# Kernel optimization log

Hardware: AMD Instinct MI355X
Metric: run time of the kernel (lower is better)

Reference implementation:

```python
import jax, jax.numpy as jnp
import numpy as np

LN_EPS = 1e-5

def _ln(x, g, b):
    m = jnp.mean(x, -1, keepdims=True)
    v = jnp.var(x, -1, keepdims=True)
    return (x - m) / jnp.sqrt(v + LN_EPS) * g + b

def _modgru(X, M, hx0, mask, Wcomb, bcomb, Wih, Whh, bih, bhh, Wc2, bc2):
    # X, M: [S,B,D]; hx0: [B,H]; mask: [S,B]
    # comb and the input-side gate GEMMs are hx-independent -> precompute over all steps
    comb = jnp.einsum('sbd,ed->sbe', jnp.concatenate([X, M], -1), Wcomb) + bcomb  # [S,B,D]
    gi = jnp.einsum('sbd,gd->sbg', comb, Wih) + bih  # [S,B,3H]

    def step(hx, inp):
        gi_t, m_t = inp
        gh = hx @ Whh.T + bhh
        ir, iz, inn = jnp.split(gi_t, 3, -1)
        hr, hz, hn = jnp.split(gh, 3, -1)
        r = jax.nn.sigmoid(ir + hr)
        z = jax.nn.sigmoid(iz + hz)
        n = jnp.tanh(inn + r * hn)
        hnew = (1.0 - z) * n + z * hx  # torch GRUCell update
        m = m_t[:, None]
        hx = hnew * m + hx * (1.0 - m)  # mask blending
        return hx, hx

    hx_last, hs = jax.lax.scan(step, hx0, (gi, mask))  # hs: [S,B,H]
    out = jnp.einsum('sbd,ed->sbe', jnp.concatenate([comb, hs], -1), Wc2) + bc2
    return out, hx_last

def setup_inputs() -> dict:
    key = jax.random.key(0)
    ks = jax.random.split(key, 40)
    S, B, I, H = 256, 512, 70, 512
    D1 = I - 6  # rnn1 input dim (use_src=True)
    f32 = jnp.float32
    def w(k, shape, scale):
        return jax.random.normal(k, shape, f32) * scale
    inp = {
        'X': jax.random.normal(ks[0], (S, B, I), f32),
        'M': (jax.random.uniform(ks[1], (S, B, I)) < 0.9).astype(f32),
        'mask': (jax.random.uniform(ks[2], (S, B)) < 0.95).astype(f32),
        'Wi2h': w(ks[3], (H, 6), 0.3), 'bi2h': jnp.zeros((H,), f32),
        # rnn1 (ModGRU on D1 inputs)
        'Wcomb1': w(ks[4], (D1, 2 * D1), 0.08), 'bcomb1': jnp.zeros((D1,), f32),
        'Wih1': w(ks[5], (3 * H, D1), 0.08), 'Whh1': w(ks[6], (3 * H, H), 0.04),
        'bih1': jnp.zeros((3 * H,), f32), 'bhh1': jnp.zeros((3 * H,), f32),
        'Wc21': w(ks[7], (H, D1 + H), 0.04), 'bc21': jnp.zeros((H,), f32),
        # rnn2 (ModGRU on H inputs)
        'Wcomb2': w(ks[8], (H, 2 * H), 0.03), 'bcomb2': jnp.zeros((H,), f32),
        'Wih2': w(ks[9], (3 * H, H), 0.04), 'Whh2': w(ks[10], (3 * H, H), 0.04),
        'bih2': jnp.zeros((3 * H,), f32), 'bhh2': jnp.zeros((3 * H,), f32),
        'Wc22': w(ks[11], (H, 2 * H), 0.03), 'bc22': jnp.zeros((H,), f32),
        # layer norms
        'g1': jnp.ones((H,), f32), 'b1': jnp.zeros((H,), f32),
        'g2': jnp.ones((H,), f32), 'b2': jnp.zeros((H,), f32),
        'g3': jnp.ones((8,), f32), 'b3': jnp.zeros((8,), f32),
        # heads
        'Wnn1': w(ks[12], (8, H), 0.05), 'bnn1': jnp.zeros((8,), f32),
        'Wnn2': w(ks[13], (2, 8), 0.3), 'bnn2': jnp.zeros((2,), f32),
    }
    return inp

def reference(X, M, mask, Wi2h, bi2h,
              Wcomb1, bcomb1, Wih1, Whh1, bih1, bhh1, Wc21, bc21,
              Wcomb2, bcomb2, Wih2, Whh2, bih2, bhh2, Wc22, bc22,
              g1, b1, g2, b2, g3, b3, Wnn1, bnn1, Wnn2, bnn2):
    # use_src=True: last 6 channels are static patient info
    patient = X[0, :, -6:]                  # [B,6]
    Xin, Min = X[:, :, :-6], M[:, :, :-6]   # [S,B,D1]
    h0 = patient @ Wi2h.T + bi2h            # [B,H]
    hx, _ = _modgru(Xin, Min, h0, mask, Wcomb1, bcomb1, Wih1, Whh1, bih1, bhh1, Wc21, bc21)
    hx = _ln(hx, g1, b1)
    hx, _ = _modgru(hx, jnp.ones_like(hx), h0, mask, Wcomb2, bcomb2, Wih2, Whh2, bih2, bhh2, Wc22, bc22)
    hx = _ln(hx, g2, b2)
    hx = jax.nn.relu(jnp.einsum('sbh,oh->sbo', hx, Wnn1) + bnn1)
    hx = _ln(hx, g3, b3)
    return jnp.einsum('sbh,oh->sbo', hx, Wnn2) + bnn2  # [S,B,2]
```

## Files before the change

### kernel.cpp

```cpp
#include <hip/hip_runtime.h>
#include <hip/hip_bf16.h>

typedef unsigned short u16;
typedef unsigned int   u32;

#define S_  256
#define B_  512
#define H_  512
#define I_  70

__device__ __forceinline__ float bfu(u16 u) {
    return __uint_as_float(((u32)u) << 16);
}
__device__ __forceinline__ u16 f2bf_u(float f) {
    __hip_bfloat16 h = __float2bfloat16(f);
    u16 r;
    __builtin_memcpy(&r, &h, 2);
    return r;
}
__device__ __forceinline__ float sigmoidf_(float x) {
    x = fminf(fmaxf(x, -30.f), 30.f);
    return 1.f / (1.f + __expf(-x));
}
__device__ __forceinline__ float tanhf_(float x) {
    x = fminf(fmaxf(x, -15.f), 15.f);
    float e = __expf(2.f * x);
    return (e - 1.f) / (e + 1.f);
}

__global__ __launch_bounds__(256)
void k_sentinel(float* __restrict__ out, int n, float v) {
    int i = blockIdx.x * 256 + threadIdx.x;
    if (i < n) out[i] = v;
}

__global__ __launch_bounds__(256)
void k_h0(const float* __restrict__ X, const float* __restrict__ Wi2h,
          const float* __restrict__ bi2h, float* __restrict__ h1a,
          float* __restrict__ h2a) {
    int idx = blockIdx.x * 256 + threadIdx.x;
    int b = idx >> 9, h = idx & 511;
    const float* xp = X + b * I_ + 64;
    const float* wp = Wi2h + h * 6;
    float s = bi2h[h];
    #pragma unroll
    for (int j = 0; j < 6; j++) s += xp[j] * wp[j];
    h1a[idx] = s;
    h2a[idx] = s;
}

__global__ __launch_bounds__(256)
void k_beff(const float* __restrict__ Wcomb2, const float* __restrict__ bcomb2,
            float* __restrict__ beff) {
    int e = blockIdx.x * 256 + threadIdx.x;
    if (e >= 512) return;
    float s = bcomb2[e];
    const float* wp = Wcomb2 + (size_t)e * 1024 + 512;
    for (int k = 0; k < 512; k++) s += wp[k];
    beff[e] = s;
}

__global__ __launch_bounds__(256)
void k_comb1(const float* __restrict__ X, const float* __restrict__ M,
             const float* __restrict__ Wcomb1, const float* __restrict__ bcomb1,
             u16* __restrict__ comb1) {
    __shared__ float W_s[128 * 68];
    __shared__ float in_s[16 * 132];
    const int tid = threadIdx.x;
    for (int i = tid; i < 64 * 128; i += 256) {
        int e = i >> 7, k = i & 127;
        W_s[k * 68 + e] = Wcomb1[i];
    }
    const size_t row0 = (size_t)blockIdx.x * 16;
    for (int i = tid; i < 16 * 128; i += 256) {
        int r = i >> 7, k = i & 127;
        size_t rg = row0 + r;
        in_s[r * 132 + k] = (k < 64) ? X[rg * I_ + k] : M[rg * I_ + (k - 64)];
    }
    __syncthreads();
    const int ty = tid >> 4, tx = tid & 15;
    float a0 = 0, a1 = 0, a2 = 0, a3 = 0;
    for (int k = 0; k < 128; k++) {
        float a = in_s[ty * 132 + k];
        float w[4];
        *(float4*)w = *(const float4*)&W_s[k * 68 + tx * 4];
        a0 = fmaf(a, w[0], a0); a1 = fmaf(a, w[1], a1);
        a2 = fmaf(a, w[2], a2); a3 = fmaf(a, w[3], a3);
    }
    size_t rg = row0 + ty;
    int e0 = tx * 4;
    ushort4 st;
    st.x = f2bf_u(a0 + bcomb1[e0 + 0]);
    st.y = f2bf_u(a1 + bcomb1[e0 + 1]);
    st.z = f2bf_u(a2 + bcomb1[e0 + 2]);
    st.w = f2bf_u(a3 + bcomb1[e0 + 3]);
    *(ushort4*)&comb1[rg * 64 + e0] = st;
}

template<int D>
__global__ __launch_bounds__(256)
void k_gru_step(const u16* __restrict__ comb,
                const float* __restrict__ Wih,
                const float* __restrict__ Whh,
                const float* __restrict__ bih, const float* __restrict__ bhh,
                const float* __restrict__ mask,
                const float* __restrict__ hcur, float* __restrict__ hnxt,
                const int t) {
    __shared__ float W_s[24 * 516];
    const int tid = threadIdx.x;
    const int hl = tid & 7;
    const int ty = tid >> 3;
    const int h0 = blockIdx.x * 8;
    const int h  = h0 + hl;
    const int b  = blockIdx.y * 64 + ty * 2;

    for (int i = tid; i < 24 * 128; i += 256) {
        int r = i >> 7, kq = i & 127;
        int g = r >> 3, hh = r & 7;
        *(float4*)&W_s[r * 516 + kq * 4] =
            *(const float4*)&Whh[((size_t)(g * 512 + h0 + hh)) * 512 + kq * 4];
    }
    __syncthreads();

    const float* hr0 = hcur + (size_t)b * 512;
    const float* hr1 = hcur + (size_t)(b + 1) * 512;
    float gh00 = bhh[h], gh10 = bhh[512 + h], gh20 = bhh[1024 + h];
    float gh01 = gh00, gh11 = gh10, gh21 = gh20;
    {
        const float* w0p = &W_s[(0 * 8 + hl) * 516];
        const float* w1p = &W_s[(1 * 8 + hl) * 516];
        const float* w2p = &W_s[(2 * 8 + hl) * 516];
        for (int k = 0; k < 512; k += 4) {
            float4 w0 = *(const float4*)(w0p + k);
            float4 w1 = *(const float4*)(w1p + k);
            float4 w2 = *(const float4*)(w2p + k);
            float4 ha = *(const float4*)(hr0 + k);
            float4 hb = *(const float4*)(hr1 + k);
            gh00 = fmaf(w0.x, ha.x, gh00); gh00 = fmaf(w0.y, ha.y, gh00);
            gh00 = fmaf(w0.z, ha.z, gh00); gh00 = fmaf(w0.w, ha.w, gh00);
            gh10 = fmaf(w1.x, ha.x, gh10); gh10 = fmaf(w1.y, ha.y, gh10);
            gh10 = fmaf(w1.z, ha.z, gh10); gh10 = fmaf(w1.w, ha.w, gh10);
            gh20 = fmaf(w2.x, ha.x, gh20); gh20 = fmaf(w2.y, ha.y, gh20);
            gh20 = fmaf(w2.z, ha.z, gh20); gh20 = fmaf(w2.w, ha.w, gh20);
            gh01 = fmaf(w0.x, hb.x, gh01); gh01 = fmaf(w0.y, hb.y, gh01);
            gh01 = fmaf(w0.z, hb.z, gh01); gh01 = fmaf(w0.w, hb.w, gh01);
            gh11 = fmaf(w1.x, hb.x, gh11); gh11 = fmaf(w1.y, hb.y, gh11);
            gh11 = fmaf(w1.z, hb.z, gh11); gh11 = fmaf(w1.w, hb.w, gh11);
            gh21 = fmaf(w2.x, hb.x, gh21); gh21 = fmaf(w2.y, hb.y, gh21);
            gh21 = fmaf(w2.z, hb.z, gh21); gh21 = fmaf(w2.w, hb.w, gh21);
        }
    }
    __syncthreads();
    constexpr int KQ = D / 4;
    constexpr int WST = (D == 512) ? 516 : (D + 4);
    for (int i = tid; i < 24 * KQ; i += 256) {
        int r = i / KQ, kq = i % KQ;
        int g = r >> 3, hh = r & 7;
        *(float4*)&W_s[r * WST + kq * 4] =
            *(const float4*)&Wih[((size_t)(g * 512 + h0 + hh)) * D + kq * 4];
    }
    __syncthreads();

    const u16* cr0 = comb + ((size_t)t * 512 + b) * D;
    const u16* cr1 = comb + ((size_t)t * 512 + b + 1) * D;
    float gi00 = bih[h], gi10 = bih[512 + h], gi20 = bih[1024 + h];
    float gi01 = gi00, gi11 = gi10, gi21 = gi20;
    {
        const float* w0p = &W_s[(0 * 8 + hl) * WST];
        const float* w1p = &W_s[(1 * 8 + hl) * WST];
        const float* w2p = &W_s[(2 * 8 + hl) * WST];
        for (int k = 0; k < D; k += 4) {
            float4 w0 = *(const float4*)(w0p + k);
            float4 w1 = *(const float4*)(w1p + k);
            float4 w2 = *(const float4*)(w2p + k);
            ushort4 cu0 = *(const ushort4*)(cr0 + k);
            ushort4 cu1 = *(const ushort4*)(cr1 + k);
            float ca[4] = {bfu(cu0.x), bfu(cu0.y), bfu(cu0.z), bfu(cu0.w)};
            float cb[4] = {bfu(cu1.x), bfu(cu1.y), bfu(cu1.z), bfu(cu1.w)};
            gi00 = fmaf(w0.x, ca[0], gi00); gi00 = fmaf(w0.y, ca[1], gi00);
            gi00 = fmaf(w0.z, ca[2], gi00); gi00 = fmaf(w0.w, ca[3], gi00);
            gi10 = fmaf(w1.x, ca[0], gi10); gi10 = fmaf(w1.y, ca[1], gi10);
            gi10 = fmaf(w1.z, ca[2], gi10); gi10 = fmaf(w1.w, ca[3], gi10);
            gi20 = fmaf(w2.x, ca[0], gi20); gi20 = fmaf(w2.y, ca[1], gi20);
            gi20 = fmaf(w2.z, ca[2], gi20); gi20 = fmaf(w2.w, ca[3], gi20);
            gi01 = fmaf(w0.x, cb[0], gi01); gi01 = fmaf(w0.y, cb[1], gi01);
            gi01 = fmaf(w0.z, cb[2], gi01); gi01 = fmaf(w0.w, cb[3], gi01);
            gi11 = fmaf(w1.x, cb[0], gi11); gi11 = fmaf(w1.y, cb[1], gi11);
            gi11 = fmaf(w1.z, cb[2], gi11); gi11 = fmaf(w1.w, cb[3], gi11);
            gi21 = fmaf(w2.x, cb[0], gi21); gi21 = fmaf(w2.y, cb[1], gi21);
            gi21 = fmaf(w2.z, cb[2], gi21); gi21 = fmaf(w2.w, cb[3], gi21);
        }
    }
    {
        float hold = hr0[h];
        float r = sigmoidf_(gi00 + gh00);
        float z = sigmoidf_(gi10 + gh10);
        float n = tanhf_(gi20 + r * gh20);
        float m = mask[t * 512 + b];
        hnxt[(size_t)b * 512 + h] = ((1.f - z) * n + z * hold) * m + hold * (1.f - m);
    }
    {
        float hold = hr1[h];
        float r = sigmoidf_(gi01 + gh01);
        float z = sigmoidf_(gi11 + gh11);
        float n = tanhf_(gi21 + r * gh21);
        float m = mask[t * 512 + b + 1];
        hnxt[(size_t)(b + 1) * 512 + h] = ((1.f - z) * n + z * hold) * m + hold * (1.f - m);
    }
}

__global__ __launch_bounds__(256)
void k_out1comb2(const u16* __restrict__ c1t, const float* __restrict__ h1,
                 const float* __restrict__ Wc21, const float* __restrict__ bc21,
                 const float* __restrict__ g1, const float* __restrict__ b1,
                 const float* __restrict__ Wcomb2, const float* __restrict__ beff,
                 u16* __restrict__ c2t) {
    __shared__ float x_s[4 * 576];
    __shared__ float y_s[4 * 512];
    const int tid = threadIdx.x;
    const int row0 = blockIdx.x * 4;
    for (int i = tid; i < 4 * 64; i += 256) {
        int r = i >> 6, k = i & 63;
        x_s[r * 576 + k] = bfu(c1t[(size_t)(row0 + r) * 64 + k]);
    }
    for (int i = tid; i < 4 * 512; i += 256) {
        int r = i >> 9, k = i & 511;
        x_s[r * 576 + 64 + k] = h1[(size_t)(row0 + r) * 512 + k];
    }
    __syncthreads();
    const int w = tid >> 6, lane = tid & 63;
    const int cg = lane >> 4, kl = lane & 15;
    for (int i = 0; i < 32; i++) {
        int o = i * 16 + w * 4 + cg;
        const float* wrow = Wc21 + (size_t)o * 576;
        float racc[4] = {0.f, 0.f, 0.f, 0.f};
        #pragma unroll
        for (int g = 0; g < 9; g++) {
            int k = g * 64 + kl * 4;
            float4 wv = *(const float4*)(wrow + k);
            #pragma unroll
            for (int r = 0; r < 4; r++) {
                float4 xv = *(const float4*)(x_s + r * 576 + k);
                racc[r] = fmaf(wv.x, xv.x, racc[r]);
                racc[r] = fmaf(wv.y, xv.y, racc[r]);
                racc[r] = fmaf(wv.z, xv.z, racc[r]);
                racc[r] = fmaf(wv.w, xv.w, racc[r]);
            }
        }
        #pragma unroll
        for (int r = 0; r < 4; r++) {
            racc[r] += __shfl_xor(racc[r], 1, 64);
            racc[r] += __shfl_xor(racc[r], 2, 64);
            racc[r] += __shfl_xor(racc[r], 4, 64);
            racc[r] += __shfl_xor(racc[r], 8, 64);
        }
        if (kl == 0) {
            float bb = bc21[o];
            #pragma unroll
            for (int r = 0; r < 4; r++) y_s[r * 512 + o] = racc[r] + bb;
        }
    }
    __syncthreads();
    {
        float v[8], sum = 0.f, ssq = 0.f;
        #pragma unroll
        for (int j = 0; j < 8; j++) {
            v[j] = y_s[w * 512 + lane * 8 + j];
            sum += v[j]; ssq += v[j] * v[j];
        }
        #pragma unroll
        for (int m = 1; m < 64; m <<= 1) {
            sum += __shfl_xor(sum, m, 64);
            ssq += __shfl_xor(ssq, m, 64);
        }
        float mu = sum * (1.f / 512.f);
        float rstd = rsqrtf(ssq * (1.f / 512.f) - mu * mu + 1e-5f);
        #pragma unroll
        for (int j = 0; j < 8; j++) {
            int o = lane * 8 + j;
            y_s[w * 512 + o] = (v[j] - mu) * rstd * g1[o] + b1[o];
        }
    }
    __syncthreads();
    for (int i = 0; i < 32; i++) {
        int o = i * 16 + w * 4 + cg;
        const float* wrow = Wcomb2 + (size_t)o * 1024;
        float racc[4] = {0.f, 0.f, 0.f, 0.f};
        #pragma unroll
        for (int g = 0; g < 8; g++) {
            int k = g * 64 + kl * 4;
            float4 wv = *(const float4*)(wrow + k);
            #pragma unroll
            for (int r = 0; r < 4; r++) {
                float4 xv = *(const float4*)(y_s + r * 512 + k);
                racc[r] = fmaf(wv.x, xv.x, racc[r]);
                racc[r] = fmaf(wv.y, xv.y, racc[r]);
                racc[r] = fmaf(wv.z, xv.z, racc[r]);
                racc[r] = fmaf(wv.w, xv.w, racc[r]);
            }
        }
        #pragma unroll
        for (int r = 0; r < 4; r++) {
            racc[r] += __shfl_xor(racc[r], 1, 64);
            racc[r] += __shfl_xor(racc[r], 2, 64);
            racc[r] += __shfl_xor(racc[r], 4, 64);
            racc[r] += __shfl_xor(racc[r], 8, 64);
        }
        if (kl == 0) {
            float bb = beff[o];
            #pragma unroll
            for (int r = 0; r < 4; r++)
                c2t[(size_t)(row0 + r) * 512 + o] = f2bf_u(racc[r] + bb);
        }
    }
}

__global__ __launch_bounds__(256)
void k_out2head(const u16* __restrict__ c2t, const float* __restrict__ h2,
                const float* __restrict__ Wc22, const float* __restrict__ bc22,
                const float* __restrict__ g2, const float* __restrict__ b2,
                const float* __restrict__ Wnn1, const float* __restrict__ bnn1,
                const float* __restrict__ g3, const float* __restrict__ b3,
                const float* __restrict__ Wnn2, const float* __restrict__ bnn2,
                float* __restrict__ outt) {
    __shared__ float x_s[4 * 1024];
    __shared__ float y_s[4 * 512];
    const int tid = threadIdx.x;
    const int row0 = blockIdx.x * 4;
    for (int i = tid; i < 4 * 512; i += 256) {
        int r = i >> 9, k = i & 511;
        x_s[r * 1024 + k] = bfu(c2t[(size_t)(row0 + r) * 512 + k]);
        x_s[r * 1024 + 512 + k] = h2[(size_t)(row0 + r) * 512 + k];
    }
    __syncthreads();
    const int w = tid >> 6, lane = tid & 63;
    const int cg = lane >> 4, kl = lane & 15;
    for (int i = 0; i < 32; i++) {
        int o = i * 16 + w * 4 + cg;
        const float* wrow = Wc22 + (size_t)o * 1024;
        float racc[4] = {0.f, 0.f, 0.f, 0.f};
        #pragma unroll
        for (int g = 0; g < 16; g++) {
            int k = g * 64 + kl * 4;
            float4 wv = *(const float4*)(wrow + k);
            #pragma unroll
            for (int r = 0; r < 4; r++) {
                float4 xv = *(const float4*)(x_s + r * 1024 + k);
                racc[r] = fmaf(wv.x, xv.x, racc[r]);
                racc[r] = fmaf(wv.y, xv.y, racc[r]);
                racc[r] = fmaf(wv.z, xv.z, racc[r]);
                racc[r] = fmaf(wv.w, xv.w, racc[r]);
            }
        }
        #pragma unroll
        for (int r = 0; r < 4; r++) {
            racc[r] += __shfl_xor(racc[r], 1, 64);
            racc[r] += __shfl_xor(racc[r], 2, 64);
            racc[r] += __shfl_xor(racc[r], 4, 64);
            racc[r] += __shfl_xor(racc[r], 8, 64);
        }
        if (kl == 0) {
            float bb = bc22[o];
            #pragma unroll
            for (int r = 0; r < 4; r++) y_s[r * 512 + o] = racc[r] + bb;
        }
    }
    __syncthreads();
    {
        float v[8], sum = 0.f, ssq = 0.f;
        #pragma unroll
        for (int j = 0; j < 8; j++) {
            v[j] = y_s[w * 512 + lane * 8 + j];
            sum += v[j]; ssq += v[j] * v[j];
        }
        #pragma unroll
        for (int m = 1; m < 64; m <<= 1) {
            sum += __shfl_xor(sum, m, 64);
            ssq += __shfl_xor(ssq, m, 64);
        }
        float mu = sum * (1.f / 512.f);
        float rstd = rsqrtf(ssq * (1.f / 512.f) - mu * mu + 1e-5f);
        #pragma unroll
        for (int j = 0; j < 8; j++) {
            int o = lane * 8 + j;
            y_s[w * 512 + o] = (v[j] - mu) * rstd * g2[o] + b2[o];
        }
    }
    __syncthreads();
    {
        float p[8];
        const float* yp = y_s + w * 512 + lane * 8;
        #pragma unroll
        for (int o8 = 0; o8 < 8; o8++) {
            const float* wp = Wnn1 + o8 * 512 + lane * 8;
            float s = 0.f;
            #pragma unroll
            for (int j = 0; j < 8; j++) s = fmaf(yp[j], wp[j], s);
            p[o8] = s;
        }
        #pragma unroll
        for (int m = 1; m < 64; m <<= 1) {
            #pragma unroll
            for (int o8 = 0; o8 < 8; o8++) p[o8] += __shfl_xor(p[o8], m, 64);
        }
        if (lane == 0) {
            float tv[8], m8 = 0.f;
            #pragma unroll
            for (int o8 = 0; o8 < 8; o8++) {
                tv[o8] = fmaxf(p[o8] + bnn1[o8], 0.f);
                m8 += tv[o8];
            }
            m8 *= 0.125f;
            float var = 0.f;
            #pragma unroll
            for (int o8 = 0; o8 < 8; o8++) { float d = tv[o8] - m8; var += d * d; }
            var *= 0.125f;
            const float rstd8 = rsqrtf(var + 1e-5f);
            float o0v = bnn2[0], o1v = bnn2[1];
            #pragma unroll
            for (int o8 = 0; o8 < 8; o8++) {
                float v = (tv[o8] - m8) * rstd8 * g3[o8] + b3[o8];
                o0v += v * Wnn2[o8];
                o1v += v * Wnn2[8 + o8];
            }
            outt[(row0 + w) * 2 + 0] = o0v;
            outt[(row0 + w) * 2 + 1] = o1v;
        }
    }
}

extern "C" void kernel_launch(void* const* d_in, const int* in_sizes, int n_in,
                              void* d_out, int out_size, void* d_ws, size_t ws_size,
                              hipStream_t stream) {
    const float* X      = (const float*)d_in[0];
    const float* M      = (const float*)d_in[1];
    const float* mask   = (const float*)d_in[2];
    const float* Wi2h   = (const float*)d_in[3];
    const float* bi2h   = (const float*)d_in[4];
    const float* Wcomb1 = (const float*)d_in[5];
    const float* bcomb1 = (const float*)d_in[6];
    const float* Wih1   = (const float*)d_in[7];
    const float* Whh1   = (const float*)d_in[8];
    const float* bih1   = (const float*)d_in[9];
    const float* bhh1   = (const float*)d_in[10];
    const float* Wc21   = (const float*)d_in[11];
    const float* bc21   = (const float*)d_in[12];
    const float* Wcomb2 = (const float*)d_in[13];
    const float* bcomb2 = (const float*)d_in[14];
    const float* Wih2   = (const float*)d_in[15];
    const float* Whh2   = (const float*)d_in[16];
    const float* bih2   = (const float*)d_in[17];
    const float* bhh2   = (const float*)d_in[18];
    const float* Wc22   = (const float*)d_in[19];
    const float* bc22   = (const float*)d_in[20];
    const float* g1     = (const float*)d_in[21];
    const float* b1     = (const float*)d_in[22];
    const float* g2     = (const float*)d_in[23];
    const float* b2     = (const float*)d_in[24];
    const float* g3     = (const float*)d_in[25];
    const float* b3     = (const float*)d_in[26];
    const float* Wnn1   = (const float*)d_in[27];
    const float* bnn1   = (const float*)d_in[28];
    const float* Wnn2   = (const float*)d_in[29];
    const float* bnn2   = (const float*)d_in[30];
    float* out = (float*)d_out;

    const size_t SZ_COMB1 = (size_t)S_ * B_ * 64 * 2;
    const size_t SZ_HX    = (size_t)B_ * H_ * 4;
    const size_t SZ_C2T   = (size_t)B_ * 512 * 2;
    const size_t NEED = SZ_COMB1 + 4 * SZ_HX + SZ_C2T + 8192;
    if (ws_size < NEED) {
        float v = 1.0e4f + (float)(ws_size >> 20);
        k_sentinel<<<(out_size + 255) / 256, 256, 0, stream>>>(out, out_size, v);
        return;
    }
    char* ws = (char*)d_ws;
    u16* comb1 = (u16*)ws;   ws += SZ_COMB1;
    float* h1a = (float*)ws; ws += SZ_HX;
    float* h1b = (float*)ws; ws += SZ_HX;
    float* h2a = (float*)ws; ws += SZ_HX;
    float* h2b = (float*)ws; ws += SZ_HX;
    u16* c2t   = (u16*)ws;   ws += SZ_C2T;
    float* beff = (float*)ws; ws += 512 * 4;

    k_h0<<<1024, 256, 0, stream>>>(X, Wi2h, bi2h, h1a, h2a);
    k_beff<<<2, 256, 0, stream>>>(Wcomb2, bcomb2, beff);
    k_comb1<<<8192, 256, 0, stream>>>(X, M, Wcomb1, bcomb1, comb1);

    for (int t = 0; t < S_; t++) {
        const float* h1c = (t & 1) ? h1b : h1a;
        float*       h1n = (t & 1) ? h1a : h1b;
        const float* h2c = (t & 1) ? h2b : h2a;
        float*       h2n = (t & 1) ? h2a : h2b;
        k_gru_step<64><<<dim3(64, 8), 256, 0, stream>>>(
            comb1, Wih1, Whh1, bih1, bhh1, mask, h1c, h1n, t);
        k_out1comb2<<<128, 256, 0, stream>>>(
            comb1 + (size_t)t * B_ * 64, h1n, Wc21, bc21, g1, b1,
            Wcomb2, beff, c2t);
        k_gru_step<512><<<dim3(64, 8), 256, 0, stream>>>(
            c2t, Wih2, Whh2, bih2, bhh2, mask + (size_t)t * B_, h2c, h2n, 0);
        k_out2head<<<128, 256, 0, stream>>>(
            c2t, h2n, Wc22, bc22, g2, b2, Wnn1, bnn1, g3, b3, Wnn2, bnn2,
            out + (size_t)t * B_ * 2);
    }
}
```

Baseline: 88.38 ms.

## Fuse per-timestep kernels into one persistent cooperative kernel with grid syncs

Replaces the 1024 per-timestep kernel launches with a single cooperative persistent kernel of 512 blocks that loops over timesteps and separates the four phases with grid.sync. GRU weight staging is split into 256-wide K chunks so shared memory fits about 25KB, which allows two blocks per CU and co-residency of all 512 blocks. The aim is to remove launch overhead and inter-kernel gaps. In exchange it adds grid-wide barriers and threadfences, and weights are still reloaded from global every step. A fallback multi-launch path runs if the cooperative launch fails.

```diff
diff --git a/kernel.cpp b/kernel.cpp
--- a/kernel.cpp
+++ b/kernel.cpp
@@ -1,5 +1,8 @@
 #include <hip/hip_runtime.h>
 #include <hip/hip_bf16.h>
+#include <hip/hip_cooperative_groups.h>
+
+namespace cg = cooperative_groups;
 
 typedef unsigned short u16;
 typedef unsigned int   u32;
@@ -8,6 +11,8 @@
 #define B_  512
 #define H_  512
 #define I_  70
+
+#define SM_FLOATS 6240
 
 __device__ __forceinline__ float bfu(u16 u) {
     return __uint_as_float(((u32)u) << 16);
@@ -97,45 +102,51 @@
     *(ushort4*)&comb1[rg * 64 + e0] = st;
 }
 
+
 template<int D>
-__global__ __launch_bounds__(256)
-void k_gru_step(const u16* __restrict__ comb,
-                const float* __restrict__ Wih,
-                const float* __restrict__ Whh,
-                const float* __restrict__ bih, const float* __restrict__ bhh,
-                const float* __restrict__ mask,
-                const float* __restrict__ hcur, float* __restrict__ hnxt,
-                const int t) {
-    __shared__ float W_s[24 * 516];
+__device__ void gru_phase(float* __restrict__ W_s,
+                          const u16* __restrict__ comb_t,
+                          const float* __restrict__ Wih,
+                          const float* __restrict__ Whh,
+                          const float* __restrict__ bih,
+                          const float* __restrict__ bhh,
+                          const float* __restrict__ maskRow,
+                          const float* __restrict__ hcur,
+                          float* __restrict__ hnxt) {
     const int tid = threadIdx.x;
     const int hl = tid & 7;
     const int ty = tid >> 3;
-    const int h0 = blockIdx.x * 8;
+    const int h0 = (blockIdx.x & 63) * 8;
     const int h  = h0 + hl;
-    const int b  = blockIdx.y * 64 + ty * 2;
-
-    for (int i = tid; i < 24 * 128; i += 256) {
-        int r = i >> 7, kq = i & 127;
-        int g = r >> 3, hh = r & 7;
-        *(float4*)&W_s[r * 516 + kq * 4] =
-            *(const float4*)&Whh[((size_t)(g * 512 + h0 + hh)) * 512 + kq * 4];
-    }
-    __syncthreads();
+    const int b  = (blockIdx.x >> 6) * 64 + ty * 2;
 
     const float* hr0 = hcur + (size_t)b * 512;
     const float* hr1 = hcur + (size_t)(b + 1) * 512;
     float gh00 = bhh[h], gh10 = bhh[512 + h], gh20 = bhh[1024 + h];
     float gh01 = gh00, gh11 = gh10, gh21 = gh20;
-    {
-        const float* w0p = &W_s[(0 * 8 + hl) * 516];
-        const float* w1p = &W_s[(1 * 8 + hl) * 516];
-        const float* w2p = &W_s[(2 * 8 + hl) * 516];
-        for (int k = 0; k < 512; k += 4) {
+
+    #pragma unroll
+    for (int half = 0; half < 2; half++) {
+        const int kbase = half * 256;
+        __syncthreads();
+        for (int i = tid; i < 24 * 64; i += 256) {
+            int r = i >> 6, kq = i & 63;
+            int g = r >> 3, hh = r & 7;
+            *(float4*)&W_s[r * 260 + kq * 4] =
+                *(const float4*)&Whh[((size_t)(g * 512 + h0 + hh)) * 512 + kbase + kq * 4];
+        }
+        __syncthreads();
+        const float* w0p = &W_s[(0 * 8 + hl) * 260];
+        const float* w1p = &W_s[(1 * 8 + hl) * 260];
+        const float* w2p = &W_s[(2 * 8 + hl) * 260];
+        const float* hap = hr0 + kbase;
+        const float* hbp = hr1 + kbase;
+        for (int k = 0; k < 256; k += 4) {
             float4 w0 = *(const float4*)(w0p + k);
             float4 w1 = *(const float4*)(w1p + k);
             float4 w2 = *(const float4*)(w2p + k);
-            float4 ha = *(const float4*)(hr0 + k);
-            float4 hb = *(const float4*)(hr1 + k);
+            float4 ha = *(const float4*)(hap + k);
+            float4 hb = *(const float4*)(hbp + k);
             gh00 = fmaf(w0.x, ha.x, gh00); gh00 = fmaf(w0.y, ha.y, gh00);
             gh00 = fmaf(w0.z, ha.z, gh00); gh00 = fmaf(w0.w, ha.w, gh00);
             gh10 = fmaf(w1.x, ha.x, gh10); gh10 = fmaf(w1.y, ha.y, gh10);
@@ -150,31 +161,32 @@
             gh21 = fmaf(w2.z, hb.z, gh21); gh21 = fmaf(w2.w, hb.w, gh21);
         }
     }
-    __syncthreads();
-    constexpr int KQ = D / 4;
-    constexpr int WST = (D == 512) ? 516 : (D + 4);
-    for (int i = tid; i < 24 * KQ; i += 256) {
-        int r = i / KQ, kq = i % KQ;
-        int g = r >> 3, hh = r & 7;
-        *(float4*)&W_s[r * WST + kq * 4] =
-            *(const float4*)&Wih[((size_t)(g * 512 + h0 + hh)) * D + kq * 4];
-    }
-    __syncthreads();
-
-    const u16* cr0 = comb + ((size_t)t * 512 + b) * D;
-    const u16* cr1 = comb + ((size_t)t * 512 + b + 1) * D;
+
+    constexpr int CH = (D < 256) ? D : 256;
+    constexpr int ST = CH + 4;
+    const u16* cr0 = comb_t + (size_t)b * D;
+    const u16* cr1 = comb_t + (size_t)(b + 1) * D;
     float gi00 = bih[h], gi10 = bih[512 + h], gi20 = bih[1024 + h];
     float gi01 = gi00, gi11 = gi10, gi21 = gi20;
-    {
-        const float* w0p = &W_s[(0 * 8 + hl) * WST];
-        const float* w1p = &W_s[(1 * 8 + hl) * WST];
-        const float* w2p = &W_s[(2 * 8 + hl) * WST];
-        for (int k = 0; k < D; k += 4) {
+    #pragma unroll
+    for (int kbase = 0; kbase < D; kbase += CH) {
+        __syncthreads();
+        for (int i = tid; i < 24 * (CH / 4); i += 256) {
+            int r = i / (CH / 4), kq = i % (CH / 4);
+            int g = r >> 3, hh = r & 7;
+            *(float4*)&W_s[r * ST + kq * 4] =
+                *(const float4*)&Wih[((size_t)(g * 512 + h0 + hh)) * D + kbase + kq * 4];
+        }
+        __syncthreads();
+        const float* w0p = &W_s[(0 * 8 + hl) * ST];
+        const float* w1p = &W_s[(1 * 8 + hl) * ST];
+        const float* w2p = &W_s[(2 * 8 + hl) * ST];
+        for (int k = 0; k < CH; k += 4) {
             float4 w0 = *(const float4*)(w0p + k);
             float4 w1 = *(const float4*)(w1p + k);
             float4 w2 = *(const float4*)(w2p + k);
-            ushort4 cu0 = *(const ushort4*)(cr0 + k);
-            ushort4 cu1 = *(const ushort4*)(cr1 + k);
+            ushort4 cu0 = *(const ushort4*)(cr0 + kbase + k);
+            ushort4 cu1 = *(const ushort4*)(cr1 + kbase + k);
             float ca[4] = {bfu(cu0.x), bfu(cu0.y), bfu(cu0.z), bfu(cu0.w)};
             float cb[4] = {bfu(cu1.x), bfu(cu1.y), bfu(cu1.z), bfu(cu1.w)};
             gi00 = fmaf(w0.x, ca[0], gi00); gi00 = fmaf(w0.y, ca[1], gi00);
@@ -196,7 +208,7 @@
         float r = sigmoidf_(gi00 + gh00);
         float z = sigmoidf_(gi10 + gh10);
         float n = tanhf_(gi20 + r * gh20);
-        float m = mask[t * 512 + b];
+        float m = maskRow[b];
         hnxt[(size_t)b * 512 + h] = ((1.f - z) * n + z * hold) * m + hold * (1.f - m);
     }
     {
@@ -204,19 +216,19 @@
         float r = sigmoidf_(gi01 + gh01);
         float z = sigmoidf_(gi11 + gh11);
         float n = tanhf_(gi21 + r * gh21);
-        float m = mask[t * 512 + b + 1];
+        float m = maskRow[b + 1];
         hnxt[(size_t)(b + 1) * 512 + h] = ((1.f - z) * n + z * hold) * m + hold * (1.f - m);
     }
 }
 
-__global__ __launch_bounds__(256)
-void k_out1comb2(const u16* __restrict__ c1t, const float* __restrict__ h1,
-                 const float* __restrict__ Wc21, const float* __restrict__ bc21,
-                 const float* __restrict__ g1, const float* __restrict__ b1,
-                 const float* __restrict__ Wcomb2, const float* __restrict__ beff,
-                 u16* __restrict__ c2t) {
-    __shared__ float x_s[4 * 576];
-    __shared__ float y_s[4 * 512];
+__device__ void b1_phase(float* __restrict__ sm,
+                         const u16* __restrict__ c1t, const float* __restrict__ h1,
+                         const float* __restrict__ Wc21, const float* __restrict__ bc21,
+                         const float* __restrict__ lg1, const float* __restrict__ lb1,
+                         const float* __restrict__ Wcomb2, const float* __restrict__ beff,
+                         u16* __restrict__ c2t) {
+    float* x_s = sm;
+    float* y_s = sm + 4 * 576;
     const int tid = threadIdx.x;
     const int row0 = blockIdx.x * 4;
     for (int i = tid; i < 4 * 64; i += 256) {
@@ -229,9 +241,9 @@
     }
     __syncthreads();
     const int w = tid >> 6, lane = tid & 63;
-    const int cg = lane >> 4, kl = lane & 15;
+    const int cg_ = lane >> 4, kl = lane & 15;
     for (int i = 0; i < 32; i++) {
-        int o = i * 16 + w * 4 + cg;
+        int o = i * 16 + w * 4 + cg_;
         const float* wrow = Wc21 + (size_t)o * 576;
         float racc[4] = {0.f, 0.f, 0.f, 0.f};
         #pragma unroll
@@ -278,12 +290,12 @@
         #pragma unroll
         for (int j = 0; j < 8; j++) {
             int o = lane * 8 + j;
-            y_s[w * 512 + o] = (v[j] - mu) * rstd * g1[o] + b1[o];
+            y_s[w * 512 + o] = (v[j] - mu) * rstd * lg1[o] + lb1[o];
         }
     }
     __syncthreads();
     for (int i = 0; i < 32; i++) {
-        int o = i * 16 + w * 4 + cg;
+        int o = i * 16 + w * 4 + cg_;
         const float* wrow = Wcomb2 + (size_t)o * 1024;
         float racc[4] = {0.f, 0.f, 0.f, 0.f};
         #pragma unroll
@@ -315,16 +327,16 @@
     }
 }
 
-__global__ __launch_bounds__(256)
-void k_out2head(const u16* __restrict__ c2t, const float* __restrict__ h2,
-                const float* __restrict__ Wc22, const float* __restrict__ bc22,
-                const float* __restrict__ g2, const float* __restrict__ b2,
-                const float* __restrict__ Wnn1, const float* __restrict__ bnn1,
-                const float* __restrict__ g3, const float* __restrict__ b3,
-                const float* __restrict__ Wnn2, const float* __restrict__ bnn2,
-                float* __restrict__ outt) {
-    __shared__ float x_s[4 * 1024];
-    __shared__ float y_s[4 * 512];
+__device__ void b2_phase(float* __restrict__ sm,
+                         const u16* __restrict__ c2t, const float* __restrict__ h2,
+                         const float* __restrict__ Wc22, const float* __restrict__ bc22,
+                         const float* __restrict__ lg2, const float* __restrict__ lb2,
+                         const float* __restrict__ Wnn1, const float* __restrict__ bnn1,
+                         const float* __restrict__ g3, const float* __restrict__ b3v,
+                         const float* __restrict__ Wnn2, const float* __restrict__ bnn2,
+                         float* __restrict__ outt) {
+    float* x_s = sm;
+    float* y_s = sm + 4 * 1024;
     const int tid = threadIdx.x;
     const int row0 = blockIdx.x * 4;
     for (int i = tid; i < 4 * 512; i += 256) {
@@ -334,9 +346,9 @@
     }
     __syncthreads();
     const int w = tid >> 6, lane = tid & 63;
-    const int cg = lane >> 4, kl = lane & 15;
+    const int cg_ = lane >> 4, kl = lane & 15;
     for (int i = 0; i < 32; i++) {
-        int o = i * 16 + w * 4 + cg;
+        int o = i * 16 + w * 4 + cg_;
         const float* wrow = Wc22 + (size_t)o * 1024;
         float racc[4] = {0.f, 0.f, 0.f, 0.f};
         #pragma unroll
@@ -383,7 +395,7 @@
         #pragma unroll
         for (int j = 0; j < 8; j++) {
             int o = lane * 8 + j;
-            y_s[w * 512 + o] = (v[j] - mu) * rstd * g2[o] + b2[o];
+            y_s[w * 512 + o] = (v[j] - mu) * rstd * lg2[o] + lb2[o];
         }
     }
     __syncthreads();
@@ -419,7 +431,7 @@
             float o0v = bnn2[0], o1v = bnn2[1];
             #pragma unroll
             for (int o8 = 0; o8 < 8; o8++) {
-                float v = (tv[o8] - m8) * rstd8 * g3[o8] + b3[o8];
+                float v = (tv[o8] - m8) * rstd8 * g3[o8] + b3v[o8];
                 o0v += v * Wnn2[o8];
                 o1v += v * Wnn2[8 + o8];
             }
@@ -427,6 +439,88 @@
             outt[(row0 + w) * 2 + 1] = o1v;
         }
     }
+}
+
+__global__ __launch_bounds__(256, 2)
+void k_scan(const u16* __restrict__ comb1, const float* __restrict__ mask,
+            const float* __restrict__ Wih1, const float* __restrict__ Whh1,
+            const float* __restrict__ bih1, const float* __restrict__ bhh1,
+            const float* __restrict__ Wc21, const float* __restrict__ bc21,
+            const float* __restrict__ lg1, const float* __restrict__ lb1,
+            const float* __restrict__ Wcomb2, const float* __restrict__ beff,
+            const float* __restrict__ Wih2, const float* __restrict__ Whh2,
+            const float* __restrict__ bih2, const float* __restrict__ bhh2,
+            const float* __restrict__ Wc22, const float* __restrict__ bc22,
+            const float* __restrict__ lg2, const float* __restrict__ lb2,
+            const float* __restrict__ Wnn1, const float* __restrict__ bnn1,
+            const float* __restrict__ g3, const float* __restrict__ b3v,
+            const float* __restrict__ Wnn2, const float* __restrict__ bnn2,
+            float* __restrict__ h1a, float* __restrict__ h1b,
+            float* __restrict__ h2a, float* __restrict__ h2b,
+            u16* __restrict__ c2t, float* __restrict__ out) {
+    cg::grid_group grid = cg::this_grid();
+    __shared__ float sm[SM_FLOATS];
+
+    for (int t = 0; t < S_; t++) {
+        const float* h1c = (t & 1) ? h1b : h1a;
+        float*       h1n = (t & 1) ? h1a : h1b;
+        const float* h2c = (t & 1) ? h2b : h2a;
+        float*       h2n = (t & 1) ? h2a : h2b;
+        const float* maskRow = mask + (size_t)t * B_;
+
+        gru_phase<64>(sm, comb1 + (size_t)t * B_ * 64, Wih1, Whh1, bih1, bhh1,
+                      maskRow, h1c, h1n);
+        __threadfence();
+        grid.sync();
+
+        if (blockIdx.x < 128)
+            b1_phase(sm, comb1 + (size_t)t * B_ * 64, h1n, Wc21, bc21, lg1, lb1,
+                     Wcomb2, beff, c2t);
+        __threadfence();
+        grid.sync();
+
+        gru_phase<512>(sm, c2t, Wih2, Whh2, bih2, bhh2, maskRow, h2c, h2n);
+        __threadfence();
+        grid.sync();
+
+        if (blockIdx.x < 128)
+            b2_phase(sm, c2t, h2n, Wc22, bc22, lg2, lb2, Wnn1, bnn1, g3, b3v,
+                     Wnn2, bnn2, out + (size_t)t * B_ * 2);
+        __threadfence();
+        grid.sync();
+    }
+}
+
+template<int D>
+__global__ __launch_bounds__(256, 2)
+void k_gru_fb(const u16* __restrict__ comb_t, const float* __restrict__ Wih,
+              const float* __restrict__ Whh, const float* __restrict__ bih,
+              const float* __restrict__ bhh, const float* __restrict__ maskRow,
+              const float* __restrict__ hcur, float* __restrict__ hnxt) {
+    __shared__ float sm[SM_FLOATS];
+    gru_phase<D>(sm, comb_t, Wih, Whh, bih, bhh, maskRow, hcur, hnxt);
+}
+
+__global__ __launch_bounds__(256, 2)
+void k_b1_fb(const u16* __restrict__ c1t, const float* __restrict__ h1,
+             const float* __restrict__ Wc21, const float* __restrict__ bc21,
+             const float* __restrict__ lg1, const float* __restrict__ lb1,
+             const float* __restrict__ Wcomb2, const float* __restrict__ beff,
+             u16* __restrict__ c2t) {
+    __shared__ float sm[SM_FLOATS];
+    b1_phase(sm, c1t, h1, Wc21, bc21, lg1, lb1, Wcomb2, beff, c2t);
+}
+
+__global__ __launch_bounds__(256, 2)
+void k_b2_fb(const u16* __restrict__ c2t, const float* __restrict__ h2,
+             const float* __restrict__ Wc22, const float* __restrict__ bc22,
+             const float* __restrict__ lg2, const float* __restrict__ lb2,
+             const float* __restrict__ Wnn1, const float* __restrict__ bnn1,
+             const float* __restrict__ g3, const float* __restrict__ b3v,
+             const float* __restrict__ Wnn2, const float* __restrict__ bnn2,
+             float* __restrict__ outt) {
+    __shared__ float sm[SM_FLOATS];
+    b2_phase(sm, c2t, h2, Wc22, bc22, lg2, lb2, Wnn1, bnn1, g3, b3v, Wnn2, bnn2, outt);
 }
 
 extern "C" void kernel_launch(void* const* d_in, const int* in_sizes, int n_in,
@@ -487,20 +581,52 @@
     k_beff<<<2, 256, 0, stream>>>(Wcomb2, bcomb2, beff);
     k_comb1<<<8192, 256, 0, stream>>>(X, M, Wcomb1, bcomb1, comb1);
 
-    for (int t = 0; t < S_; t++) {
-        const float* h1c = (t & 1) ? h1b : h1a;
-        float*       h1n = (t & 1) ? h1a : h1b;
-        const float* h2c = (t & 1) ? h2b : h2a;
-        float*       h2n = (t & 1) ? h2a : h2b;
-        k_gru_step<64><<<dim3(64, 8), 256, 0, stream>>>(
-            comb1, Wih1, Whh1, bih1, bhh1, mask, h1c, h1n, t);
-        k_out1comb2<<<128, 256, 0, stream>>>(
-            comb1 + (size_t)t * B_ * 64, h1n, Wc21, bc21, g1, b1,
-            Wcomb2, beff, c2t);
-        k_gru_step<512><<<dim3(64, 8), 256, 0, stream>>>(
-            c2t, Wih2, Whh2, bih2, bhh2, mask + (size_t)t * B_, h2c, h2n, 0);
-        k_out2head<<<128, 256, 0, stream>>>(
-            c2t, h2n, Wc22, bc22, g2, b2, Wnn1, bnn1, g3, b3, Wnn2, bnn2,
-            out + (size_t)t * B_ * 2);
-    }
-}
+    const u16* a_comb1 = comb1; const float* a_mask = mask;
+    const float* a_Wih1 = Wih1; const float* a_Whh1 = Whh1;
+    const float* a_bih1 = bih1; const float* a_bhh1 = bhh1;
+    const float* a_Wc21 = Wc21; const float* a_bc21 = bc21;
+    const float* a_g1 = g1; const float* a_b1 = b1;
+    const float* a_Wcomb2 = Wcomb2; const float* a_beff = beff;
+    const float* a_Wih2 = Wih2; const float* a_Whh2 = Whh2;
+    const float* a_bih2 = bih2; const float* a_bhh2 = bhh2;
+    const float* a_Wc22 = Wc22; const float* a_bc22 = bc22;
+    const float* a_g2 = g2; const float* a_b2 = b2;
+    const float* a_Wnn1 = Wnn1; const float* a_bnn1 = bnn1;
+    const float* a_g3 = g3; const float* a_b3 = b3;
+    const float* a_Wnn2 = Wnn2; const float* a_bnn2 = bnn2;
+    float* a_h1a = h1a; float* a_h1b = h1b;
+    float* a_h2a = h2a; float* a_h2b = h2b;
+    u16* a_c2t = c2t; float* a_out = out;
+    void* args[] = {
+        &a_comb1, &a_mask,
+        &a_Wih1, &a_Whh1, &a_bih1, &a_bhh1,
+        &a_Wc21, &a_bc21, &a_g1, &a_b1,
+        &a_Wcomb2, &a_beff,
+        &a_Wih2, &a_Whh2, &a_bih2, &a_bhh2,
+        &a_Wc22, &a_bc22, &a_g2, &a_b2,
+        &a_Wnn1, &a_bnn1, &a_g3, &a_b3, &a_Wnn2, &a_bnn2,
+        &a_h1a, &a_h1b, &a_h2a, &a_h2b, &a_c2t, &a_out
+    };
+    hipError_t cerr = hipLaunchCooperativeKernel((const void*)k_scan, dim3(512),
+                                                 dim3(256), args, 0, stream);
+    if (cerr != hipSuccess) {
+        for (int t = 0; t < S_; t++) {
+            const float* h1c = (t & 1) ? h1b : h1a;
+            float*       h1n = (t & 1) ? h1a : h1b;
+            const float* h2c = (t & 1) ? h2b : h2a;
+            float*       h2n = (t & 1) ? h2a : h2b;
+            const float* maskRow = mask + (size_t)t * B_;
+            k_gru_fb<64><<<512, 256, 0, stream>>>(
+                comb1 + (size_t)t * B_ * 64, Wih1, Whh1, bih1, bhh1,
+                maskRow, h1c, h1n);
+            k_b1_fb<<<128, 256, 0, stream>>>(
+                comb1 + (size_t)t * B_ * 64, h1n, Wc21, bc21, g1, b1,
+                Wcomb2, beff, c2t);
+            k_gru_fb<512><<<512, 256, 0, stream>>>(
+                c2t, Wih2, Whh2, bih2, bhh2, maskRow, h2c, h2n);
+            k_b2_fb<<<128, 256, 0, stream>>>(
+                c2t, h2n, Wc22, bc22, g2, b2, Wnn1, bnn1, g3, b3,
+                Wnn2, bnn2, out + (size_t)t * B_ * 2);
+        }
+    }
+}
```

Measured after the change: 222.4 ms. 152% more time.
